# Kernel optimization log

Hardware: AMD Instinct MI355X
Metric: run time of the kernel (lower is better)

The kernel has to match this reference:

```python
import jax, jax.numpy as jnp
import numpy as np

B, H, S, D = 4, 16, 1024, 64

def setup_inputs() -> dict:
    key = jax.random.key(0)
    kq, kk, kv, kb, km = jax.random.split(key, 5)
    return {
        "q": jax.random.normal(kq, (B, H, S, D), dtype=jnp.float32),
        "k": jax.random.normal(kk, (B, H, S, D), dtype=jnp.float32),
        "v": jax.random.normal(kv, (B, H, S, D), dtype=jnp.float32),
        "add_attn": jax.random.normal(kb, (B, 1, S, S), dtype=jnp.float32),
        "mask": jax.random.randint(km, (B, 1, 1, S), 0, 2, dtype=jnp.int32),
    }

def reference(q, k, v, add_attn, mask):
    d_emb = q.shape[-1]
    scale = 1.0 / jnp.sqrt(jnp.float32(d_emb)).astype(q.dtype)
    # scores: [B,H,Sq,Sk]
    attn = jnp.einsum('bhqd,bhkd->bhqk', q * scale, k)
    attn = attn + add_attn
    attn = jnp.where(mask == 0, jnp.asarray(-1e9, attn.dtype), attn)
    attn = jax.nn.softmax(attn, axis=-1)  # dropout with p=0 is identity
    output = jnp.einsum('bhqk,bhkd->bhqd', attn, v)
    return (output, attn)
```

## Files before the change

kernel.cpp:

```cpp
#include <hip/hip_runtime.h>
#include <math.h>

#define BB 4
#define HH 16
#define SS 1024
#define DD 64
#define QT 16
#define NKW 4
#define KPW 256
#define HPB 4
#define OSTR 66

typedef __attribute__((ext_vector_type(8))) short bf16x8;
typedef __attribute__((ext_vector_type(4))) float f32x4;

static __device__ inline unsigned short f2bf(float f) {
    unsigned int u = __float_as_uint(f);
    u += 0x7fff + ((u >> 16) & 1);
    return (unsigned short)(u >> 16);
}

__global__ __launch_bounds__(256) void convert_qk(const float* __restrict__ q,
                                                  const float* __restrict__ k,
                                                  unsigned short* __restrict__ qb,
                                                  unsigned short* __restrict__ kb) {
    const int idx = blockIdx.x * 256 + threadIdx.x;
    float4 qv = ((const float4*)q)[idx];
    float4 kv = ((const float4*)k)[idx];
    ushort4 qo = make_ushort4(f2bf(qv.x), f2bf(qv.y), f2bf(qv.z), f2bf(qv.w));
    ushort4 ko = make_ushort4(f2bf(kv.x), f2bf(kv.y), f2bf(kv.z), f2bf(kv.w));
    ((ushort4*)qb)[idx] = qo;
    ((ushort4*)kb)[idx] = ko;
}

__global__ __launch_bounds__(256) void transpose_v(const float* __restrict__ v,
                                                   unsigned short* __restrict__ vt) {
    __shared__ unsigned short t[DD][258];
    const int bh = blockIdx.y;
    const int k0 = blockIdx.x * 256;
    const float* vb = v + ((size_t)bh * SS + k0) * DD;
#pragma unroll
    for (int j = 0; j < 16; ++j) {
        const int f   = j * 256 + threadIdx.x;
        const int row = f >> 4;
        const int d4  = (f & 15) << 2;
        float4 x = ((const float4*)vb)[f];
        t[d4 + 0][row] = f2bf(x.x);
        t[d4 + 1][row] = f2bf(x.y);
        t[d4 + 2][row] = f2bf(x.z);
        t[d4 + 3][row] = f2bf(x.w);
    }
    __syncthreads();
    unsigned short* vo = vt + (size_t)bh * DD * SS + k0;
#pragma unroll
    for (int j = 0; j < 8; ++j) {
        const int f  = j * 256 + threadIdx.x;
        const int d  = f >> 5;
        const int k8 = (f & 31) << 3;
        const unsigned int* lp = (const unsigned int*)&t[d][k8];
        uint4 w;
        w.x = lp[0]; w.y = lp[1]; w.z = lp[2]; w.w = lp[3];
        *(uint4*)(vo + (size_t)d * SS + k8) = w;
    }
}

__global__ __launch_bounds__(256, 2) void attn_mfma(
    const unsigned short* __restrict__ qb,
    const unsigned short* __restrict__ kb,
    const unsigned short* __restrict__ vtb,
    const float* __restrict__ add_attn,
    const int*   __restrict__ mask,
    float* __restrict__ out,
    float* __restrict__ attn_out)
{
    const int P    = blockIdx.x;
    const int xcd  = P & 7;
    const int slot = P >> 3;
    const int hg   = slot & 3;
    const int g    = ((slot >> 2) << 3) | xcd;
    const int qt   = g & 63;
    const int b    = g >> 6;

    const int tid = threadIdx.x;
    const int wave = tid >> 6;
    const int lane = tid & 63;
    const int col  = lane & 15;
    const int quad = lane >> 4;

    __shared__ unsigned short p_tile[NKW][QT][KPW + 8];
    __shared__ float red_m[NKW][QT];
    __shared__ float red_l[NKW][QT];
    float* o_w = (float*)&p_tile[wave][0][0];

    const int q0  = qt * QT;
    const int wk0 = wave * KPW;

    const float* bias = add_attn + ((size_t)b * SS + q0) * SS;
    const int*   mrow = mask + b * SS;
    float br[16][4];
#pragma unroll
    for (int t = 0; t < 16; ++t) {
        const int kidx = wk0 + t * 16 + col;
        const int mv = mrow[kidx];
#pragma unroll
        for (int r = 0; r < 4; ++r) {
            const int qr = quad * 4 + r;
            float bv = bias[(size_t)qr * SS + kidx];
            br[t][r] = mv ? bv : -1e9f;
        }
    }

    for (int hi = 0; hi < HPB; ++hi) {
        const int h  = hg * HPB + hi;
        const int bh = b * HH + h;

        const unsigned short* qrow = qb + ((size_t)bh * SS + q0 + col) * DD + quad * 8;
        const bf16x8 aq0 = *(const bf16x8*)(qrow);
        const bf16x8 aq1 = *(const bf16x8*)(qrow + 32);

        const unsigned short* kbb = kb + (size_t)bh * SS * DD;

        float s[16][4];
#pragma unroll
        for (int t = 0; t < 16; ++t) {
            const int k0 = wk0 + t * 16;
            const unsigned short* kr = kbb + (size_t)(k0 + col) * DD + quad * 8;
            bf16x8 bk0 = *(const bf16x8*)(kr);
            bf16x8 bk1 = *(const bf16x8*)(kr + 32);
            f32x4 acc = {0.f, 0.f, 0.f, 0.f};
            acc = __builtin_amdgcn_mfma_f32_16x16x32_bf16(aq0, bk0, acc, 0, 0, 0);
            acc = __builtin_amdgcn_mfma_f32_16x16x32_bf16(aq1, bk1, acc, 0, 0, 0);
#pragma unroll
            for (int r = 0; r < 4; ++r)
                s[t][r] = acc[r] * 0.125f + br[t][r];
        }

        float mx[4];
#pragma unroll
        for (int r = 0; r < 4; ++r) {
            float m = s[0][r];
#pragma unroll
            for (int t = 1; t < 16; ++t) m = fmaxf(m, s[t][r]);
            m = fmaxf(m, __shfl_xor(m, 1));
            m = fmaxf(m, __shfl_xor(m, 2));
            m = fmaxf(m, __shfl_xor(m, 4));
            m = fmaxf(m, __shfl_xor(m, 8));
            mx[r] = m;
        }
        if (col == 0) {
#pragma unroll
            for (int r = 0; r < 4; ++r) red_m[wave][quad * 4 + r] = mx[r];
        }
        __syncthreads();
        float mf[4];
#pragma unroll
        for (int r = 0; r < 4; ++r) {
            const int qr = quad * 4 + r;
            mf[r] = fmaxf(fmaxf(red_m[0][qr], red_m[1][qr]),
                          fmaxf(red_m[2][qr], red_m[3][qr]));
        }

        float ls[4] = {0.f, 0.f, 0.f, 0.f};
#pragma unroll
        for (int t = 0; t < 16; ++t) {
#pragma unroll
            for (int r = 0; r < 4; ++r) {
                float e = __expf(s[t][r] - mf[r]);
                s[t][r] = e;
                ls[r] += e;
            }
        }
#pragma unroll
        for (int r = 0; r < 4; ++r) {
            float l = ls[r];
            l += __shfl_xor(l, 1);
            l += __shfl_xor(l, 2);
            l += __shfl_xor(l, 4);
            l += __shfl_xor(l, 8);
            ls[r] = l;
        }
        if (col == 0) {
#pragma unroll
            for (int r = 0; r < 4; ++r) red_l[wave][quad * 4 + r] = ls[r];
        }
        __syncthreads();
        float inv[4];
#pragma unroll
        for (int r = 0; r < 4; ++r) {
            const int qr = quad * 4 + r;
            inv[r] = 1.0f / (red_l[0][qr] + red_l[1][qr] + red_l[2][qr] + red_l[3][qr]);
        }

        float* arow = attn_out + ((size_t)bh * SS + q0) * SS;
#pragma unroll
        for (int t = 0; t < 16; ++t) {
#pragma unroll
            for (int r = 0; r < 4; ++r) {
                const int qr = quad * 4 + r;
                float p = s[t][r] * inv[r];
                arow[(size_t)qr * SS + wk0 + t * 16 + col] = p;
                p_tile[wave][qr][t * 16 + col] = f2bf(p);
            }
        }

        const unsigned short* vt = vtb + (size_t)bh * DD * SS;
        f32x4 oacc[4];
#pragma unroll
        for (int dc = 0; dc < 4; ++dc) oacc[dc] = (f32x4){0.f, 0.f, 0.f, 0.f};
#pragma unroll
        for (int c = 0; c < 8; ++c) {
            bf16x8 ap = *(const bf16x8*)(&p_tile[wave][col][c * 32 + quad * 8]);
#pragma unroll
            for (int dc = 0; dc < 4; ++dc) {
                const unsigned short* vr =
                    vt + (size_t)(dc * 16 + col) * SS + wk0 + c * 32 + quad * 8;
                bf16x8 bv = *(const bf16x8*)(vr);
                oacc[dc] = __builtin_amdgcn_mfma_f32_16x16x32_bf16(ap, bv, oacc[dc], 0, 0, 0);
            }
        }
#pragma unroll
        for (int dc = 0; dc < 4; ++dc)
#pragma unroll
            for (int r = 0; r < 4; ++r)
                o_w[(quad * 4 + r) * OSTR + dc * 16 + col] = oacc[dc][r];
        __syncthreads();

        for (int i = tid; i < QT * DD; i += 256) {
            const int qr = i >> 6, d = i & 63;
            float ov = ((const float*)&p_tile[0][0][0])[qr * OSTR + d] +
                       ((const float*)&p_tile[1][0][0])[qr * OSTR + d] +
                       ((const float*)&p_tile[2][0][0])[qr * OSTR + d] +
                       ((const float*)&p_tile[3][0][0])[qr * OSTR + d];
            out[((size_t)bh * SS + q0 + qr) * DD + d] = ov;
        }
        __syncthreads();
    }
}

extern "C" void kernel_launch(void* const* d_in, const int* in_sizes, int n_in,
                              void* d_out, int out_size, void* d_ws, size_t ws_size,
                              hipStream_t stream) {
    const float* q        = (const float*)d_in[0];
    const float* k        = (const float*)d_in[1];
    const float* v        = (const float*)d_in[2];
    const float* add_attn = (const float*)d_in[3];
    const int*   mask     = (const int*)d_in[4];

    float* out      = (float*)d_out;
    float* attn_out = (float*)d_out + (size_t)BB * HH * SS * DD;

    const size_t nelem = (size_t)BB * HH * SS * DD;
    unsigned short* qb  = (unsigned short*)d_ws;
    unsigned short* kbb = qb + nelem;
    unsigned short* vtb = kbb + nelem;

    convert_qk<<<dim3(nelem / 4 / 256), dim3(256), 0, stream>>>(q, k, qb, kbb);
    transpose_v<<<dim3(SS / 256, BB * HH), dim3(256), 0, stream>>>(v, vtb);

    attn_mfma<<<dim3(SS / QT * (HH / HPB) * BB), dim3(256), 0, stream>>>(
        qb, kbb, vtb, add_attn, mask, out, attn_out);
}
```

Before: 455.4 us.

## Transpose MFMA operands so each lane owns a query row, vectorizing stores

The MFMA operand order is swapped in both the QK^T and PV products, so each lane's accumulator holds four consecutive keys (or head-dim entries) for a single query row. This lets the bias, mask, attention-probability and output stores become 16-byte vector accesses instead of scalar strided ones. The softmax is reorganised to compute a per-wave local max and sum together and combine them across waves with online rescaling, which removes one __syncthreads per head. The exchange is extra exp calls in the cross-wave merge and a changed LDS layout that could introduce bank conflicts on the packed p_tile writes.

```diff
diff --git a/kernel.cpp b/kernel.cpp
--- a/kernel.cpp
+++ b/kernel.cpp
@@ -9,10 +9,12 @@
 #define NKW 4
 #define KPW 256
 #define HPB 4
-#define OSTR 66
+#define PTL 264
+#define OSTR 68
 
 typedef __attribute__((ext_vector_type(8))) short bf16x8;
 typedef __attribute__((ext_vector_type(4))) float f32x4;
+typedef __attribute__((ext_vector_type(4))) int   i32x4;
 
 static __device__ inline unsigned short f2bf(float f) {
     unsigned int u = __float_as_uint(f);
@@ -81,13 +83,13 @@
     const int qt   = g & 63;
     const int b    = g >> 6;
 
-    const int tid = threadIdx.x;
+    const int tid  = threadIdx.x;
     const int wave = tid >> 6;
     const int lane = tid & 63;
     const int col  = lane & 15;
     const int quad = lane >> 4;
 
-    __shared__ unsigned short p_tile[NKW][QT][KPW + 8];
+    __shared__ unsigned short p_tile[NKW][QT][PTL];
     __shared__ float red_m[NKW][QT];
     __shared__ float red_l[NKW][QT];
     float* o_w = (float*)&p_tile[wave][0][0];
@@ -95,112 +97,87 @@
     const int q0  = qt * QT;
     const int wk0 = wave * KPW;
 
-    const float* bias = add_attn + ((size_t)b * SS + q0) * SS;
+    const float* brow = add_attn + ((size_t)b * SS + q0 + col) * SS;
     const int*   mrow = mask + b * SS;
     float br[16][4];
 #pragma unroll
     for (int t = 0; t < 16; ++t) {
-        const int kidx = wk0 + t * 16 + col;
-        const int mv = mrow[kidx];
-#pragma unroll
-        for (int r = 0; r < 4; ++r) {
-            const int qr = quad * 4 + r;
-            float bv = bias[(size_t)qr * SS + kidx];
-            br[t][r] = mv ? bv : -1e9f;
-        }
+        const int kof = wk0 + t * 16 + quad * 4;
+        const f32x4 bv = *(const f32x4*)(brow + kof);
+        const i32x4 mv = *(const i32x4*)(mrow + kof);
+#pragma unroll
+        for (int r = 0; r < 4; ++r)
+            br[t][r] = mv[r] ? bv[r] : -1e9f;
     }
 
     for (int hi = 0; hi < HPB; ++hi) {
-        const int h  = hg * HPB + hi;
-        const int bh = b * HH + h;
+        const int bh = b * HH + hg * HPB + hi;
 
         const unsigned short* qrow = qb + ((size_t)bh * SS + q0 + col) * DD + quad * 8;
-        const bf16x8 aq0 = *(const bf16x8*)(qrow);
-        const bf16x8 aq1 = *(const bf16x8*)(qrow + 32);
+        const bf16x8 bq0 = *(const bf16x8*)(qrow);
+        const bf16x8 bq1 = *(const bf16x8*)(qrow + 32);
 
         const unsigned short* kbb = kb + (size_t)bh * SS * DD;
 
         float s[16][4];
 #pragma unroll
         for (int t = 0; t < 16; ++t) {
-            const int k0 = wk0 + t * 16;
-            const unsigned short* kr = kbb + (size_t)(k0 + col) * DD + quad * 8;
-            bf16x8 bk0 = *(const bf16x8*)(kr);
-            bf16x8 bk1 = *(const bf16x8*)(kr + 32);
+            const unsigned short* kr = kbb + (size_t)(wk0 + t * 16 + col) * DD + quad * 8;
+            bf16x8 ak0 = *(const bf16x8*)(kr);
+            bf16x8 ak1 = *(const bf16x8*)(kr + 32);
             f32x4 acc = {0.f, 0.f, 0.f, 0.f};
-            acc = __builtin_amdgcn_mfma_f32_16x16x32_bf16(aq0, bk0, acc, 0, 0, 0);
-            acc = __builtin_amdgcn_mfma_f32_16x16x32_bf16(aq1, bk1, acc, 0, 0, 0);
+            acc = __builtin_amdgcn_mfma_f32_16x16x32_bf16(ak0, bq0, acc, 0, 0, 0);
+            acc = __builtin_amdgcn_mfma_f32_16x16x32_bf16(ak1, bq1, acc, 0, 0, 0);
 #pragma unroll
             for (int r = 0; r < 4; ++r)
                 s[t][r] = acc[r] * 0.125f + br[t][r];
         }
 
-        float mx[4];
-#pragma unroll
-        for (int r = 0; r < 4; ++r) {
-            float m = s[0][r];
-#pragma unroll
-            for (int t = 1; t < 16; ++t) m = fmaxf(m, s[t][r]);
-            m = fmaxf(m, __shfl_xor(m, 1));
-            m = fmaxf(m, __shfl_xor(m, 2));
-            m = fmaxf(m, __shfl_xor(m, 4));
-            m = fmaxf(m, __shfl_xor(m, 8));
-            mx[r] = m;
-        }
-        if (col == 0) {
-#pragma unroll
-            for (int r = 0; r < 4; ++r) red_m[wave][quad * 4 + r] = mx[r];
-        }
+        float m = s[0][0];
+#pragma unroll
+        for (int t = 0; t < 16; ++t)
+#pragma unroll
+            for (int r = 0; r < 4; ++r) m = fmaxf(m, s[t][r]);
+        m = fmaxf(m, __shfl_xor(m, 16));
+        m = fmaxf(m, __shfl_xor(m, 32));
+
+        float l = 0.f;
+#pragma unroll
+        for (int t = 0; t < 16; ++t)
+#pragma unroll
+            for (int r = 0; r < 4; ++r) {
+                float e = __expf(s[t][r] - m);
+                s[t][r] = e;
+                l += e;
+            }
+        l += __shfl_xor(l, 16);
+        l += __shfl_xor(l, 32);
+
+        if (quad == 0) { red_m[wave][col] = m; red_l[wave][col] = l; }
         __syncthreads();
-        float mf[4];
-#pragma unroll
-        for (int r = 0; r < 4; ++r) {
-            const int qr = quad * 4 + r;
-            mf[r] = fmaxf(fmaxf(red_m[0][qr], red_m[1][qr]),
-                          fmaxf(red_m[2][qr], red_m[3][qr]));
-        }
-
-        float ls[4] = {0.f, 0.f, 0.f, 0.f};
+
+        const float m0 = red_m[0][col], m1 = red_m[1][col];
+        const float m2 = red_m[2][col], m3 = red_m[3][col];
+        const float gm = fmaxf(fmaxf(m0, m1), fmaxf(m2, m3));
+        const float L  = red_l[0][col] * __expf(m0 - gm) +
+                         red_l[1][col] * __expf(m1 - gm) +
+                         red_l[2][col] * __expf(m2 - gm) +
+                         red_l[3][col] * __expf(m3 - gm);
+        const float sc = __expf(m - gm) / L;
+
+        float* arow = attn_out + ((size_t)bh * SS + q0 + col) * SS + wk0;
 #pragma unroll
         for (int t = 0; t < 16; ++t) {
+            f32x4 pv;
+            ushort4 pk;
 #pragma unroll
             for (int r = 0; r < 4; ++r) {
-                float e = __expf(s[t][r] - mf[r]);
-                s[t][r] = e;
-                ls[r] += e;
+                float p = s[t][r] * sc;
+                pv[r] = p;
+                ((unsigned short*)&pk)[r] = f2bf(p);
             }
-        }
-#pragma unroll
-        for (int r = 0; r < 4; ++r) {
-            float l = ls[r];
-            l += __shfl_xor(l, 1);
-            l += __shfl_xor(l, 2);
-            l += __shfl_xor(l, 4);
-            l += __shfl_xor(l, 8);
-            ls[r] = l;
-        }
-        if (col == 0) {
-#pragma unroll
-            for (int r = 0; r < 4; ++r) red_l[wave][quad * 4 + r] = ls[r];
-        }
-        __syncthreads();
-        float inv[4];
-#pragma unroll
-        for (int r = 0; r < 4; ++r) {
-            const int qr = quad * 4 + r;
-            inv[r] = 1.0f / (red_l[0][qr] + red_l[1][qr] + red_l[2][qr] + red_l[3][qr]);
-        }
-
-        float* arow = attn_out + ((size_t)bh * SS + q0) * SS;
-#pragma unroll
-        for (int t = 0; t < 16; ++t) {
-#pragma unroll
-            for (int r = 0; r < 4; ++r) {
-                const int qr = quad * 4 + r;
-                float p = s[t][r] * inv[r];
-                arow[(size_t)qr * SS + wk0 + t * 16 + col] = p;
-                p_tile[wave][qr][t * 16 + col] = f2bf(p);
-            }
+            *(f32x4*)(arow + t * 16 + quad * 4) = pv;
+            *(ushort4*)&p_tile[wave][col][t * 16 + quad * 4] = pk;
         }
 
         const unsigned short* vt = vtb + (size_t)bh * DD * SS;
@@ -214,24 +191,26 @@
             for (int dc = 0; dc < 4; ++dc) {
                 const unsigned short* vr =
                     vt + (size_t)(dc * 16 + col) * SS + wk0 + c * 32 + quad * 8;
-                bf16x8 bv = *(const bf16x8*)(vr);
-                oacc[dc] = __builtin_amdgcn_mfma_f32_16x16x32_bf16(ap, bv, oacc[dc], 0, 0, 0);
+                bf16x8 av = *(const bf16x8*)(vr);
+                oacc[dc] = __builtin_amdgcn_mfma_f32_16x16x32_bf16(av, ap, oacc[dc], 0, 0, 0);
             }
         }
 #pragma unroll
         for (int dc = 0; dc < 4; ++dc)
-#pragma unroll
-            for (int r = 0; r < 4; ++r)
-                o_w[(quad * 4 + r) * OSTR + dc * 16 + col] = oacc[dc][r];
+            *(f32x4*)(o_w + col * OSTR + dc * 16 + quad * 4) = oacc[dc];
         __syncthreads();
 
-        for (int i = tid; i < QT * DD; i += 256) {
-            const int qr = i >> 6, d = i & 63;
-            float ov = ((const float*)&p_tile[0][0][0])[qr * OSTR + d] +
-                       ((const float*)&p_tile[1][0][0])[qr * OSTR + d] +
-                       ((const float*)&p_tile[2][0][0])[qr * OSTR + d] +
-                       ((const float*)&p_tile[3][0][0])[qr * OSTR + d];
-            out[((size_t)bh * SS + q0 + qr) * DD + d] = ov;
+        {
+            const int qr = tid >> 4;
+            const int d0 = (tid & 15) << 2;
+            const float* ob = (const float*)&p_tile[0][0][0];
+            const int ws = QT * PTL / 2;
+            f32x4 a0 = *(const f32x4*)(ob + 0 * ws + qr * OSTR + d0);
+            f32x4 a1 = *(const f32x4*)(ob + 1 * ws + qr * OSTR + d0);
+            f32x4 a2 = *(const f32x4*)(ob + 2 * ws + qr * OSTR + d0);
+            f32x4 a3 = *(const f32x4*)(ob + 3 * ws + qr * OSTR + d0);
+            f32x4 o4 = a0 + a1 + a2 + a3;
+            *(f32x4*)(out + ((size_t)bh * SS + q0 + qr) * DD + d0) = o4;
         }
         __syncthreads();
     }
```

Measured after the change: 465.9 us. 1.02x slower.
